# Performance work log

Hardware: AMD Instinct MI355X
Metric: run time of the kernel (lower is better)

The kernel has to match this reference:

```python
import jax, jax.numpy as jnp
import numpy as np
from jax import lax

B, H, W, C = 4, 128, 128, 192
HEADS = 4
CH = C // HEADS  # head dim = 48


def setup_inputs() -> dict:
    key = jax.random.key(0)
    ks = jax.random.split(key, 5)
    x = jax.random.normal(ks[0], (B, H, W, C), dtype=jnp.float32)
    # 1x1 conv producing qkv: stored as dense [C, 3C]
    w_qkv = jax.random.normal(ks[1], (C, 3 * C), dtype=jnp.float32) * (1.0 / np.sqrt(C))
    # depthwise 3x3 conv over 3C channels: HWIO with I=1, O=3C, feature_group_count=3C
    w_dw = jax.random.normal(ks[2], (3, 3, 1, 3 * C), dtype=jnp.float32) * (1.0 / 3.0)
    # output projection 1x1 conv: dense [C, C]
    w_proj = jax.random.normal(ks[3], (C, C), dtype=jnp.float32) * (1.0 / np.sqrt(C))
    # per-head learned temperature (initialized to ones as in the source)
    temperature = jnp.ones((HEADS,), dtype=jnp.float32)
    return {"x": x, "w_qkv": w_qkv, "w_dw": w_dw, "w_proj": w_proj, "temperature": temperature}


def _l2_normalize(t):
    # tf.keras.utils.normalize: divide by L2 norm along last axis
    return t / jnp.linalg.norm(t, axis=-1, keepdims=True)


def reference(x, w_qkv, w_dw, w_proj, temperature):
    b, h, w, c = x.shape
    hw = h * w
    # 1x1 conv == dense matmul over channels
    qkv = jnp.einsum('bhwc,cd->bhwd', x, w_qkv)  # [b,h,w,3C]
    # depthwise 3x3 SAME conv
    qkv = lax.conv_general_dilated(
        qkv, w_dw, window_strides=(1, 1), padding='SAME',
        dimension_numbers=('NHWC', 'HWIO', 'NHWC'),
        feature_group_count=3 * c)
    q, k, v = jnp.split(qkv, 3, axis=-1)  # each [b,h,w,C]

    def to_heads(t):
        # b h w (heads ch) -> b heads ch (h w)
        return t.reshape(b, hw, HEADS, CH).transpose(0, 2, 3, 1)

    q = _l2_normalize(to_heads(q))  # [b,heads,ch,hw]
    k = _l2_normalize(to_heads(k))
    v = to_heads(v)

    temp = temperature.reshape(1, HEADS, 1, 1)
    attn = jnp.einsum('bncs,bnds->bncd', q, k) * temp  # [b,heads,ch,ch]
    attn = jax.nn.softmax(attn, axis=-1)
    out = jnp.einsum('bncd,bnds->bncs', attn, v)  # [b,heads,ch,hw]
    # b heads ch (h w) -> b h w (heads ch)
    out = out.transpose(0, 3, 1, 2).reshape(b, h, w, c)
    out = jnp.einsum('bhwc,cd->bhwd', out, w_proj)
    return out
```

## Files before the change

### kernel.cpp

```cpp
#include <hip/hip_runtime.h>

namespace {

constexpr int HW = 16384;
constexpr int C  = 192;
constexpr int C3 = 576;
constexpr int CH = 48;
constexpr int K  = 192;

using bf16x8 = __attribute__((ext_vector_type(8))) short;
using f32x4  = __attribute__((ext_vector_type(4))) float;

__device__ inline unsigned short f2bf(float f) {
  unsigned u = __float_as_uint(f);
  unsigned r = (u + 0x7fff + ((u >> 16) & 1)) >> 16;
  return (unsigned short)r;
}
__device__ inline float bf2f(unsigned short b) {
  return __uint_as_float(((unsigned)b) << 16);
}
__device__ inline float4 ld_bf4(const unsigned short* p) {
  const ushort4 u = *(const ushort4*)p;
  return make_float4(bf2f(u.x), bf2f(u.y), bf2f(u.z), bf2f(u.w));
}

__device__ __forceinline__ void ld_g2l16(const unsigned short* g, unsigned short* l) {
  __builtin_amdgcn_global_load_lds(
      (const __attribute__((address_space(1))) unsigned int*)(unsigned long long)(const void*)g,
      (__attribute__((address_space(3))) unsigned int*)(unsigned int)(unsigned long long)(void*)l,
      16, 0, 0);
}

__global__ __launch_bounds__(256) void cvt_wqkv(const float* __restrict__ wqkv,
                                                unsigned short* __restrict__ wqh) {
  const int t = blockIdx.x * 256 + threadIdx.x;
  const int n = t / 192;
  const int k = t % 192;
  wqh[n * 192 + k] = f2bf(wqkv[k * C3 + n]);
}

template <int NT, bool PERB, bool OBF16, bool CVTA, bool TWOB>
__global__ __launch_bounds__(256) void gemm_mfma(const void* __restrict__ Ap,
                                                 const unsigned short* __restrict__ Bh,
                                                 const unsigned short* __restrict__ Bl,
                                                 void* __restrict__ Co) {
  constexpr int N = NT * 64;
  constexpr int AST = CVTA ? 40 : 32;
  __shared__ __align__(16) unsigned short sA[128 * AST];
  __shared__ __align__(16) unsigned short sBh[2][2][64 * 32];
  __shared__ __align__(16) unsigned short sBl[TWOB ? 2 : 1][TWOB ? 2 : 1][TWOB ? 64 * 32 : 8];
  const int t = threadIdx.x;
  const int lane = t & 63;
  const int wv = t >> 6;
  const int m0 = blockIdx.x * 128;
  const size_t boff = PERB ? (size_t)(m0 >> 14) * (192 * 192) : 0;
  const int wr = wv >> 1, wc = wv & 1;
  const int fr_row = lane & 15;
  const int fr_swz = ((lane >> 4) ^ (lane & 3)) << 3;
  const int arow0 = wv * 32;
  const int lrow  = lane >> 2;
  const int lslot = lane & 3;
  const int brow0 = wv * 16;
  const int ssl   = lslot ^ (lrow & 3);

  bf16x8 fah[6][4];
#pragma unroll
  for (int ks = 0; ks < 6; ++ks) {
    const int k0 = ks * 32;
#pragma unroll
    for (int r = 0; r < 2; ++r) {
      const int row = arow0 + r * 16 + lrow;
      if constexpr (CVTA) {
        const float* src = &((const float*)Ap)[(size_t)(m0 + row) * K + k0 + (lslot << 3)];
        const float4 f0 = *(const float4*)src;
        const float4 f1 = *(const float4*)(src + 4);
        bf16x8 h;
        h[0] = (short)f2bf(f0.x); h[1] = (short)f2bf(f0.y);
        h[2] = (short)f2bf(f0.z); h[3] = (short)f2bf(f0.w);
        h[4] = (short)f2bf(f1.x); h[5] = (short)f2bf(f1.y);
        h[6] = (short)f2bf(f1.z); h[7] = (short)f2bf(f1.w);
        const int sphys = lslot ^ (row & 3);
        *(bf16x8*)&sA[row * AST + (sphys << 3)] = h;
      } else {
        const size_t go = (size_t)(m0 + row) * K + k0 + ((lslot ^ (row & 3)) << 3);
        ld_g2l16(&((const unsigned short*)Ap)[go], &sA[(arow0 + r * 16) * AST]);
      }
    }
    __syncthreads();
#pragma unroll
    for (int i = 0; i < 4; ++i) {
      const int row = wr * 64 + i * 16 + fr_row;
      fah[ks][i] = *(const bf16x8*)&sA[row * AST + fr_swz];
    }
    __syncthreads();
  }

  auto stageB = [&](int buf, int nt_, int kp_) {
#pragma unroll
    for (int s = 0; s < 2; ++s) {
      const size_t go = boff + (size_t)(nt_ * 64 + brow0 + lrow) * K
                      + kp_ * 64 + s * 32 + (ssl << 3);
      ld_g2l16(&Bh[go], &sBh[buf][s][brow0 * 32]);
      if constexpr (TWOB) ld_g2l16(&Bl[go], &sBl[buf][s][brow0 * 32]);
    }
  };

  stageB(0, 0, 0);
  __syncthreads();
  const int er = (lane >> 4) << 2;
  const int ec = lane & 15;
  for (int nt = 0; nt < NT; ++nt) {
    f32x4 acc[4][2] = {};
#pragma unroll
    for (int kp = 0; kp < 3; ++kp) {
      const int buf = (nt + kp) & 1;
      const bool last = (nt == NT - 1) && (kp == 2);
      if (!last) {
        if (kp < 2) stageB(buf ^ 1, nt, kp + 1);
        else        stageB(buf ^ 1, nt + 1, 0);
      }
#pragma unroll
      for (int sub = 0; sub < 2; ++sub) {
        const int ks = kp * 2 + sub;
        bf16x8 fbh[2];
#pragma unroll
        for (int j = 0; j < 2; ++j) {
          const int row = wc * 32 + j * 16 + fr_row;
          fbh[j] = *(const bf16x8*)&sBh[buf][sub][row * 32 + fr_swz];
        }
#pragma unroll
        for (int i = 0; i < 4; ++i)
#pragma unroll
          for (int j = 0; j < 2; ++j)
            acc[i][j] = __builtin_amdgcn_mfma_f32_16x16x32_bf16(fah[ks][i], fbh[j], acc[i][j], 0, 0, 0);
        if constexpr (TWOB) {
          bf16x8 fbl[2];
#pragma unroll
          for (int j = 0; j < 2; ++j) {
            const int row = wc * 32 + j * 16 + fr_row;
            fbl[j] = *(const bf16x8*)&sBl[buf][sub][row * 32 + fr_swz];
          }
#pragma unroll
          for (int i = 0; i < 4; ++i)
#pragma unroll
            for (int j = 0; j < 2; ++j)
              acc[i][j] = __builtin_amdgcn_mfma_f32_16x16x32_bf16(fah[ks][i], fbl[j], acc[i][j], 0, 0, 0);
        }
      }
      if (!last) __syncthreads();
    }
#pragma unroll
    for (int i = 0; i < 4; ++i)
#pragma unroll
      for (int j = 0; j < 2; ++j) {
        const size_t base = (size_t)(m0 + wr * 64 + i * 16 + er) * N + nt * 64 + wc * 32 + j * 16 + ec;
        if constexpr (OBF16) {
          unsigned short* cp = (unsigned short*)Co + base;
#pragma unroll
          for (int r = 0; r < 4; ++r) cp[(size_t)r * N] = f2bf(acc[i][j][r]);
        } else {
          float* cp = (float*)Co + base;
#pragma unroll
          for (int r = 0; r < 4; ++r) cp[(size_t)r * N] = acc[i][j][r];
        }
      }
  }
}

constexpr int TY = 8;
__global__ __launch_bounds__(256) void dwconv3x3_v5(const unsigned short* __restrict__ in,
                                                    const float* __restrict__ wdw,
                                                    unsigned short* __restrict__ qk,
                                                    unsigned short* __restrict__ vh) {
  const int t = blockIdx.x * 256 + threadIdx.x;
  const int c4 = t % 144;
  const int rest = t / 144;
  const int x = rest & 127;
  const int ys = (rest >> 7) & 15;
  const int img = rest >> 11;
  const int y0 = ys * TY;

  float4 wt[3][3];
#pragma unroll
  for (int i = 0; i < 3; ++i)
#pragma unroll
    for (int j = 0; j < 3; ++j)
      wt[i][j] = *(const float4*)&wdw[(size_t)(i * 3 + j) * C3 + c4 * 4];

  const bool xm = x > 0, xp = x < 127;
  const unsigned short* ibase = &in[((size_t)((img << 14) + x)) * C3 + c4 * 4];
  const float4 z4 = make_float4(0.f, 0.f, 0.f, 0.f);
  const ptrdiff_t dxm = xm ? -(ptrdiff_t)C3 : 0;
  const ptrdiff_t dxp = xp ? (ptrdiff_t)C3 : 0;

  auto ldrow = [&](int yy, float4* r) {
    if ((unsigned)yy < 128u) {
      const unsigned short* rp = ibase + (size_t)yy * (128 * C3);
      float4 a = ld_bf4(rp + dxm);
      float4 m = ld_bf4(rp);
      float4 b = ld_bf4(rp + dxp);
      if (!xm) a = z4;
      if (!xp) b = z4;
      r[0] = a; r[1] = m; r[2] = b;
    } else {
      r[0] = z4; r[1] = z4; r[2] = z4;
    }
  };

  float4 r0[3], r1[3], r2[3], rn[3];
  ldrow(y0 - 1, r0);
  ldrow(y0, r1);
  ldrow(y0 + 1, r2);

#pragma unroll
  for (int i = 0; i < TY; ++i) {
    if (i < TY - 1) ldrow(y0 + i + 2, rn);
    float4 o = z4;
#pragma unroll
    for (int j = 0; j < 3; ++j) {
      o.x += r0[j].x * wt[0][j].x; o.y += r0[j].y * wt[0][j].y;
      o.z += r0[j].z * wt[0][j].z; o.w += r0[j].w * wt[0][j].w;
      o.x += r1[j].x * wt[1][j].x; o.y += r1[j].y * wt[1][j].y;
      o.z += r1[j].z * wt[1][j].z; o.w += r1[j].w * wt[1][j].w;
      o.x += r2[j].x * wt[2][j].x; o.y += r2[j].y * wt[2][j].y;
      o.z += r2[j].z * wt[2][j].z; o.w += r2[j].w * wt[2][j].w;
    }
    const int p = (img << 14) + ((y0 + i) << 7) + x;
    const ushort4 ob = make_ushort4(f2bf(o.x), f2bf(o.y), f2bf(o.z), f2bf(o.w));
    if (c4 < 96) *(ushort4*)&qk[(size_t)p * 384 + c4 * 4] = ob;
    else         *(ushort4*)&vh[(size_t)p * 192 + (c4 - 96) * 4] = ob;
    if (i < TY - 1) {
#pragma unroll
      for (int j = 0; j < 3; ++j) { r0[j] = r1[j]; r1[j] = r2[j]; r2[j] = rn[j]; }
    }
  }
}

__global__ __launch_bounds__(256) void gram48_v4(const unsigned short* __restrict__ qk,
                                                 float* __restrict__ G,
                                                 float* __restrict__ ssqq,
                                                 float* __restrict__ ssqk) {
  constexpr int W = 50;
  __shared__ unsigned int smem[9216];
  const int tid = threadIdx.x;
  const int lane = tid & 63;
  const int wv = tid >> 6;
  const int pair = blockIdx.y;
  const int img = pair >> 2, h = pair & 3;

  f32x4 acc[3][3] = {};
  float ssq_acc = 0.f;
  const int sch = tid % 96;
  const int shalf = tid / 96;

  for (int rnd = 0; rnd < 2; ++rnd) {
    const int sbase = (img << 14) + blockIdx.x * 256 + rnd * 128;
#pragma unroll
    for (int r = 0; r < 6; ++r) {
      const int idx = tid + (r << 8);
      const int row = idx / 12, part = idx % 12;
      const bool isq = part < 6;
      const int sub = isq ? part : part - 6;
      const uint4 v = *(const uint4*)&qk[(size_t)(sbase + row) * 384 + (isq ? 0 : 192) + h * 48 + sub * 8];
      *(uint4*)&smem[row * W + (isq ? 0 : 24) + sub * 4] = v;
    }
    __syncthreads();
    {
      const int s0 = wv * 32 + ((lane >> 4) << 3);
      const int cm = lane & 15;
      const int half = cm & 1;
      bf16x8 qf[3], kf[3];
#pragma unroll
      for (int t3 = 0; t3 < 3; ++t3) {
        const int qc = t3 * 8 + (cm >> 1);
#pragma unroll
        for (int j = 0; j < 8; ++j) {
          const unsigned uq = smem[(s0 + j) * W + qc];
          const unsigned uk = smem[(s0 + j) * W + 24 + qc];
          qf[t3][j] = (short)(half ? (uq >> 16) : (uq & 0xffffu));
          kf[t3][j] = (short)(half ? (uk >> 16) : (uk & 0xffffu));
        }
      }
#pragma unroll
      for (int mt = 0; mt < 3; ++mt)
#pragma unroll
        for (int nt = 0; nt < 3; ++nt)
          acc[mt][nt] = __builtin_amdgcn_mfma_f32_16x16x32_bf16(qf[mt], kf[nt], acc[mt][nt], 0, 0, 0);
    }
    if (tid < 192) {
      const int cu = (sch < 48) ? (sch >> 1) : 24 + ((sch - 48) >> 1);
      const int hf = sch & 1;
      const int sstart = shalf * 64;
#pragma unroll 4
      for (int s = 0; s < 64; ++s) {
        const unsigned u = smem[(sstart + s) * W + cu];
        const float v = bf2f((unsigned short)(hf ? (u >> 16) : (u & 0xffffu)));
        ssq_acc += v * v;
      }
    }
    __syncthreads();
  }

  float* red = (float*)smem;
  const int col = lane & 15;
  const int rbase = (lane >> 4) * 4;
#pragma unroll
  for (int mt = 0; mt < 3; ++mt)
#pragma unroll
    for (int nt = 0; nt < 3; ++nt)
#pragma unroll
      for (int rg = 0; rg < 4; ++rg)
        red[wv * 2304 + (mt * 16 + rbase + rg) * 48 + nt * 16 + col] = acc[mt][nt][rg];
  __syncthreads();
  float* Gm = &G[(size_t)pair * 2304];
#pragma unroll
  for (int c = 0; c < 9; ++c) {
    const int cell = tid + (c << 8);
    const float s4 = red[cell] + red[2304 + cell] + red[4608 + cell] + red[6912 + cell];
    atomicAdd(&Gm[cell], s4);
  }
  if (tid < 192) {
    if (sch < 48) atomicAdd(&ssqq[img * 192 + h * 48 + sch], ssq_acc);
    else          atomicAdd(&ssqk[img * 192 + h * 48 + sch - 48], ssq_acc);
  }
}

__global__ __launch_bounds__(64) void attn_softmax(const float* __restrict__ G,
                                                   const float* __restrict__ ssqq,
                                                   const float* __restrict__ ssqk,
                                                   const float* __restrict__ temp,
                                                   float* __restrict__ attn) {
  const int r = blockIdx.x;
  const int h = blockIdx.y & 3;
  const int img = blockIdx.y >> 2;
  const int lane = threadIdx.x;
  const size_t base = (size_t)(img * 4 + h) * 2304;
  const float t = temp[h];
  const float qn = ssqq[img * 192 + h * CH + r];
  float val = -1e30f;
  if (lane < 48) {
    const float kn = ssqk[img * 192 + h * CH + lane];
    val = G[base + r * 48 + lane] * t * rsqrtf(qn * kn);
  }
  float m = val;
#pragma unroll
  for (int off = 32; off; off >>= 1) m = fmaxf(m, __shfl_xor(m, off));
  const float e = (lane < 48) ? expf(val - m) : 0.f;
  float ssum = e;
#pragma unroll
  for (int off = 32; off; off >>= 1) ssum += __shfl_xor(ssum, off);
  if (lane < 48) attn[base + r * 48 + lane] = e / ssum;
}

__global__ __launch_bounds__(256) void make_weff(const float* __restrict__ attn,
                                                 const float* __restrict__ wproj,
                                                 unsigned short* __restrict__ weh,
                                                 unsigned short* __restrict__ wel) {
  const int t = blockIdx.x * 256 + threadIdx.x;
  const int img = t / 36864;
  const int r = t % 36864;
  const int n = r / 192;
  const int D = r % 192;
  const int h = D / 48, dd = D % 48;
  const float* A = &attn[(size_t)(img * 4 + h) * 2304 + dd];
  const float* Wp = &wproj[(size_t)(h * 48) * 192 + n];
  float acc = 0.f;
#pragma unroll
  for (int c = 0; c < 48; ++c) acc += A[c * 48] * Wp[c * 192];
  const unsigned short hb = f2bf(acc);
  weh[(size_t)img * 36864 + n * 192 + D] = hb;
  wel[(size_t)img * 36864 + n * 192 + D] = f2bf(acc - bf2f(hb));
}

}

extern "C" void kernel_launch(void* const* d_in, const int* in_sizes, int n_in,
                              void* d_out, int out_size, void* d_ws, size_t ws_size,
                              hipStream_t stream) {
  const float* x      = (const float*)d_in[0];
  const float* w_qkv  = (const float*)d_in[1];
  const float* w_dw   = (const float*)d_in[2];
  const float* w_proj = (const float*)d_in[3];
  const float* temp   = (const float*)d_in[4];
  float* out = (float*)d_out;

  auto layout_bytes = [](int NI) -> size_t {
    return (size_t)NI * HW * 576 * 2
         + (size_t)NI * HW * 384 * 2
         + (size_t)NI * HW * 192 * 2
         + 221184
         + 153600
         + 147456
         + 2 * 294912;
  };
  const int NI = (ws_size >= layout_bytes(4)) ? 4 : ((ws_size >= layout_bytes(2)) ? 2 : 1);
  const int npass = 4 / NI;
  const int npix = NI * HW;

  char* p = (char*)d_ws;
  unsigned short* qkv = (unsigned short*)p; p += (size_t)npix * 576 * 2;
  unsigned short* qk = (unsigned short*)p;  p += (size_t)npix * 384 * 2;
  unsigned short* vh = (unsigned short*)p;  p += (size_t)npix * 192 * 2;
  unsigned short* wqh = (unsigned short*)p; p += 221184;
  float* G    = (float*)p;           p += 147456;
  float* ssqq = (float*)p;           p += 3072;
  float* ssqk = (float*)p;           p += 3072;
  float* attnb = (float*)p;          p += 147456;
  unsigned short* weh = (unsigned short*)p; p += 294912;
  unsigned short* wel = (unsigned short*)p;

  cvt_wqkv<<<432, 256, 0, stream>>>(w_qkv, wqh);
  hipMemsetAsync(G, 0, 153600, stream);

  for (int pass = 0; pass < npass; ++pass) {
    const float* xb = x + (size_t)pass * npix * K;
    float* outb = out + (size_t)pass * npix * C;
    float* Gp    = G + (size_t)pass * NI * 4 * 2304;
    float* sqp   = ssqq + (size_t)pass * NI * 192;
    float* skp   = ssqk + (size_t)pass * NI * 192;
    float* ap    = attnb + (size_t)pass * NI * 4 * 2304;
    unsigned short* wehp = weh + (size_t)pass * NI * 36864;
    unsigned short* welp = wel + (size_t)pass * NI * 36864;
    gemm_mfma<9, false, true, true, false><<<npix / 128, 256, 0, stream>>>(
        xb, wqh, wqh, qkv);
    dwconv3x3_v5<<<npix * 144 / TY / 256, 256, 0, stream>>>(qkv, w_dw, qk, vh);
    gram48_v4<<<dim3(64, 4 * NI), 256, 0, stream>>>(qk, Gp, sqp, skp);
    attn_softmax<<<dim3(48, 4 * NI), 64, 0, stream>>>(Gp, sqp, skp, temp, ap);
    make_weff<<<NI * 144, 256, 0, stream>>>(ap, w_proj, wehp, welp);
    gemm_mfma<3, true, false, false, true><<<npix / 128, 256, 0, stream>>>(
        vh, wehp, welp, outb);
  }
}
```

Before: 127.5 us.

## Drop bf16 hi/lo split of effective projection weight and stage full-K B tiles

The effective output-projection weight is now stored as a single bf16 array instead of a high/low bf16 pair, which halves the MFMA work and B-operand traffic in the final GEMM. The GEMM B staging now loads all six K-slices of a 64-column tile per step with double buffering across N tiles. This cuts the barriers per N tile from three to one. The cost is lower precision in the projection weights and more LDS per block (48 KB for B), which may lower occupancy.

```diff
diff --git a/kernel.cpp b/kernel.cpp
--- a/kernel.cpp
+++ b/kernel.cpp
@@ -39,16 +39,14 @@
   wqh[n * 192 + k] = f2bf(wqkv[k * C3 + n]);
 }
 
-template <int NT, bool PERB, bool OBF16, bool CVTA, bool TWOB>
+template <int NT, bool PERB, bool OBF16, bool CVTA>
 __global__ __launch_bounds__(256) void gemm_mfma(const void* __restrict__ Ap,
                                                  const unsigned short* __restrict__ Bh,
-                                                 const unsigned short* __restrict__ Bl,
                                                  void* __restrict__ Co) {
   constexpr int N = NT * 64;
   constexpr int AST = CVTA ? 40 : 32;
   __shared__ __align__(16) unsigned short sA[128 * AST];
-  __shared__ __align__(16) unsigned short sBh[2][2][64 * 32];
-  __shared__ __align__(16) unsigned short sBl[TWOB ? 2 : 1][TWOB ? 2 : 1][TWOB ? 64 * 32 : 8];
+  __shared__ __align__(16) unsigned short sB[2][6][64 * 32];
   const int t = threadIdx.x;
   const int lane = t & 63;
   const int wv = t >> 6;
@@ -95,59 +93,35 @@
     __syncthreads();
   }
 
-  auto stageB = [&](int buf, int nt_, int kp_) {
-#pragma unroll
-    for (int s = 0; s < 2; ++s) {
-      const size_t go = boff + (size_t)(nt_ * 64 + brow0 + lrow) * K
-                      + kp_ * 64 + s * 32 + (ssl << 3);
-      ld_g2l16(&Bh[go], &sBh[buf][s][brow0 * 32]);
-      if constexpr (TWOB) ld_g2l16(&Bl[go], &sBl[buf][s][brow0 * 32]);
+  auto stageB = [&](int buf, int nt_) {
+#pragma unroll
+    for (int s = 0; s < 6; ++s) {
+      const size_t go = boff + (size_t)(nt_ * 64 + brow0 + lrow) * K + s * 32 + (ssl << 3);
+      ld_g2l16(&Bh[go], &sB[buf][s][brow0 * 32]);
     }
   };
 
-  stageB(0, 0, 0);
+  stageB(0, 0);
   __syncthreads();
   const int er = (lane >> 4) << 2;
   const int ec = lane & 15;
   for (int nt = 0; nt < NT; ++nt) {
+    const int buf = nt & 1;
+    if (nt < NT - 1) stageB(buf ^ 1, nt + 1);
     f32x4 acc[4][2] = {};
 #pragma unroll
-    for (int kp = 0; kp < 3; ++kp) {
-      const int buf = (nt + kp) & 1;
-      const bool last = (nt == NT - 1) && (kp == 2);
-      if (!last) {
-        if (kp < 2) stageB(buf ^ 1, nt, kp + 1);
-        else        stageB(buf ^ 1, nt + 1, 0);
+    for (int ks = 0; ks < 6; ++ks) {
+      bf16x8 fbh[2];
+#pragma unroll
+      for (int j = 0; j < 2; ++j) {
+        const int row = wc * 32 + j * 16 + fr_row;
+        fbh[j] = *(const bf16x8*)&sB[buf][ks][row * 32 + fr_swz];
       }
 #pragma unroll
-      for (int sub = 0; sub < 2; ++sub) {
-        const int ks = kp * 2 + sub;
-        bf16x8 fbh[2];
-#pragma unroll
-        for (int j = 0; j < 2; ++j) {
-          const int row = wc * 32 + j * 16 + fr_row;
-          fbh[j] = *(const bf16x8*)&sBh[buf][sub][row * 32 + fr_swz];
-        }
-#pragma unroll
-        for (int i = 0; i < 4; ++i)
-#pragma unroll
-          for (int j = 0; j < 2; ++j)
-            acc[i][j] = __builtin_amdgcn_mfma_f32_16x16x32_bf16(fah[ks][i], fbh[j], acc[i][j], 0, 0, 0);
-        if constexpr (TWOB) {
-          bf16x8 fbl[2];
-#pragma unroll
-          for (int j = 0; j < 2; ++j) {
-            const int row = wc * 32 + j * 16 + fr_row;
-            fbl[j] = *(const bf16x8*)&sBl[buf][sub][row * 32 + fr_swz];
-          }
-#pragma unroll
-          for (int i = 0; i < 4; ++i)
-#pragma unroll
-            for (int j = 0; j < 2; ++j)
-              acc[i][j] = __builtin_amdgcn_mfma_f32_16x16x32_bf16(fah[ks][i], fbl[j], acc[i][j], 0, 0, 0);
-        }
-      }
-      if (!last) __syncthreads();
+      for (int i = 0; i < 4; ++i)
+#pragma unroll
+        for (int j = 0; j < 2; ++j)
+          acc[i][j] = __builtin_amdgcn_mfma_f32_16x16x32_bf16(fah[ks][i], fbh[j], acc[i][j], 0, 0, 0);
     }
 #pragma unroll
     for (int i = 0; i < 4; ++i)
@@ -164,6 +138,7 @@
           for (int r = 0; r < 4; ++r) cp[(size_t)r * N] = acc[i][j][r];
         }
       }
+    if (nt < NT - 1) __syncthreads();
   }
 }
 
@@ -354,8 +329,7 @@
 
 __global__ __launch_bounds__(256) void make_weff(const float* __restrict__ attn,
                                                  const float* __restrict__ wproj,
-                                                 unsigned short* __restrict__ weh,
-                                                 unsigned short* __restrict__ wel) {
+                                                 unsigned short* __restrict__ weh) {
   const int t = blockIdx.x * 256 + threadIdx.x;
   const int img = t / 36864;
   const int r = t % 36864;
@@ -367,9 +341,7 @@
   float acc = 0.f;
 #pragma unroll
   for (int c = 0; c < 48; ++c) acc += A[c * 48] * Wp[c * 192];
-  const unsigned short hb = f2bf(acc);
-  weh[(size_t)img * 36864 + n * 192 + D] = hb;
-  wel[(size_t)img * 36864 + n * 192 + D] = f2bf(acc - bf2f(hb));
+  weh[(size_t)img * 36864 + n * 192 + D] = f2bf(acc);
 }
 
 }
@@ -391,7 +363,7 @@
          + 221184
          + 153600
          + 147456
-         + 2 * 294912;
+         + 294912;
   };
   const int NI = (ws_size >= layout_bytes(4)) ? 4 : ((ws_size >= layout_bytes(2)) ? 2 : 1);
   const int npass = 4 / NI;
@@ -406,8 +378,7 @@
   float* ssqq = (float*)p;           p += 3072;
   float* ssqk = (float*)p;           p += 3072;
   float* attnb = (float*)p;          p += 147456;
-  unsigned short* weh = (unsigned short*)p; p += 294912;
-  unsigned short* wel = (unsigned short*)p;
+  unsigned short* weh = (unsigned short*)p;
 
   cvt_wqkv<<<432, 256, 0, stream>>>(w_qkv, wqh);
   hipMemsetAsync(G, 0, 153600, stream);
@@ -420,14 +391,13 @@
     float* skp   = ssqk + (size_t)pass * NI * 192;
     float* ap    = attnb + (size_t)pass * NI * 4 * 2304;
     unsigned short* wehp = weh + (size_t)pass * NI * 36864;
-    unsigned short* welp = wel + (size_t)pass * NI * 36864;
-    gemm_mfma<9, false, true, true, false><<<npix / 128, 256, 0, stream>>>(
-        xb, wqh, wqh, qkv);
+    gemm_mfma<9, false, true, true><<<npix / 128, 256, 0, stream>>>(
+        xb, wqh, qkv);
     dwconv3x3_v5<<<npix * 144 / TY / 256, 256, 0, stream>>>(qkv, w_dw, qk, vh);
     gram48_v4<<<dim3(64, 4 * NI), 256, 0, stream>>>(qk, Gp, sqp, skp);
     attn_softmax<<<dim3(48, 4 * NI), 64, 0, stream>>>(Gp, sqp, skp, temp, ap);
-    make_weff<<<NI * 144, 256, 0, stream>>>(ap, w_proj, wehp, welp);
-    gemm_mfma<3, true, false, false, true><<<npix / 128, 256, 0, stream>>>(
-        vh, wehp, welp, outb);
-  }
-}
+    make_weff<<<NI * 144, 256, 0, stream>>>(ap, w_proj, wehp);
+    gemm_mfma<3, true, false, false><<<npix / 128, 256, 0, stream>>>(
+        vh, wehp, outb);
+  }
+}
```

After: 122.2 us. 1.04x faster.
